# Performance work log

Hardware: AMD Instinct MI355X
Metric: run time of the kernel (lower is better)

Reference implementation:

```python
import jax, jax.numpy as jnp
import numpy as np

T, D, H = 65536, 256, 256


def setup_inputs() -> dict:
    key = jax.random.key(0)
    ks = jax.random.split(key, 6)
    lim = 1.0 / np.sqrt(H)  # equinox GRUCell init: U(-1/sqrt(hidden), 1/sqrt(hidden))
    x = jax.random.normal(ks[0], (T, D), dtype=jnp.float32)
    state = jnp.zeros((H,), dtype=jnp.float32)
    start = jax.random.randint(ks[1], (T,), 0, 2).astype(jnp.int32)  # episode-start mask
    next_done = jnp.zeros((T,), dtype=jnp.int32)  # unused by forward, kept for signature fidelity
    W_ih = jax.random.uniform(ks[2], (3 * H, D), minval=-lim, maxval=lim, dtype=jnp.float32)
    W_hh = jax.random.uniform(ks[3], (3 * H, H), minval=-lim, maxval=lim, dtype=jnp.float32)
    bias = jax.random.uniform(ks[4], (3 * H,), minval=-lim, maxval=lim, dtype=jnp.float32)
    bias_n = jax.random.uniform(ks[5], (H,), minval=-lim, maxval=lim, dtype=jnp.float32)
    return {"x": x, "state": state, "start": start, "next_done": next_done,
            "W_ih": W_ih, "W_hh": W_hh, "bias": bias, "bias_n": bias_n}


def reference(x, state, start, next_done, W_ih, W_hh, bias, bias_n):
    # Input-dependent gate pre-activations for all timesteps in one big GEMM: [T, 3H]
    igates_all = x @ W_ih.T + bias
    start_f = start.astype(x.dtype)

    def step(h, inp):
        ig, s = inp
        h = h * (1.0 - s)  # reset hidden at episode start (state * logical_not(start))
        hg = W_hh @ h  # [3H]
        r = jax.nn.sigmoid(ig[:H] + hg[:H])
        z = jax.nn.sigmoid(ig[H:2 * H] + hg[H:2 * H])
        n = jnp.tanh(ig[2 * H:] + r * (hg[2 * H:] + bias_n))
        new_h = n + z * (h - n)  # equinox GRUCell output
        return new_h, new_h

    final_state, y = jax.lax.scan(step, state, (igates_all, start_f))
    return y, final_state
```

## Files before the change

kernel.cpp:

```cpp
#include <hip/hip_runtime.h>
#include <hip/hip_bf16.h>
#include <stdint.h>

#define TT   65536
#define NCH  16
#define CNOM 16
#define NBLK 256
#define ROWB 1664

typedef __bf16 bf16x8 __attribute__((ext_vector_type(8)));
typedef float  f32x4  __attribute__((ext_vector_type(4)));
typedef int    i32x4  __attribute__((ext_vector_type(4)));

__device__ __bf16 g_wih[768 * 256];
__device__ __bf16 g_whh[768 * 256];
__device__ __bf16 g_xbf[TT * 256];
__device__ __align__(64) unsigned char g_ig[(size_t)TT * ROWB];

__device__ __forceinline__ void gl_lds16(const void* g, void* l) {
  __builtin_amdgcn_global_load_lds(
      (const __attribute__((address_space(1))) void*)(unsigned long long)(uintptr_t)g,
      (__attribute__((address_space(3))) void*)(unsigned int)(uintptr_t)l,
      16, 0, 0);
}

__device__ __forceinline__ bf16x8 as_bf16x8(i32x4 v) {
  bf16x8 r; __builtin_memcpy(&r, &v, 16); return r;
}
__device__ __forceinline__ float bfbits(uint32_t u) {
  float f; __builtin_memcpy(&f, &u, 4); return f;
}

__global__ void prep_w(const float* __restrict__ wih, const float* __restrict__ whh) {
  const int n = 768 * 256;
  for (int i = blockIdx.x * blockDim.x + threadIdx.x; i < n; i += gridDim.x * blockDim.x) {
    g_wih[i] = (__bf16)wih[i];
    g_whh[i] = (__bf16)whh[i];
  }
}

__global__ void prep_x(const float* __restrict__ x) {
  int i = (blockIdx.x * 256 + threadIdx.x) * 8;
  float4 a0 = *(const float4*)(x + i);
  float4 a1 = *(const float4*)(x + i + 4);
  bf16x8 v;
  v[0] = (__bf16)a0.x; v[1] = (__bf16)a0.y; v[2] = (__bf16)a0.z; v[3] = (__bf16)a0.w;
  v[4] = (__bf16)a1.x; v[5] = (__bf16)a1.y; v[6] = (__bf16)a1.z; v[7] = (__bf16)a1.w;
  *(bf16x8*)(g_xbf + i) = v;
}

__global__ __launch_bounds__(256) void gemm_ig(const float* __restrict__ bias) {
  __shared__ __align__(16) __bf16 a_s[128 * 64];
  __shared__ __align__(16) __bf16 b_s[128 * 64];
  const int tid = threadIdx.x;
  const int w = tid >> 6, lane = tid & 63, l15 = lane & 15, q = lane >> 4;
  const int mt = blockIdx.x / 6, ntb = blockIdx.x - mt * 6;
  const int m0 = mt * 128, n0 = ntb * 128;
  const int wm = w >> 1, wn = w & 1;

  f32x4 acc[4][4];
#pragma unroll
  for (int a = 0; a < 4; ++a)
#pragma unroll
    for (int b = 0; b < 4; ++b) acc[a][b] = (f32x4){0.f, 0.f, 0.f, 0.f};

  for (int kc = 0; kc < 4; ++kc) {
#pragma unroll
    for (int i = 0; i < 4; ++i) {
      int pslot = i * 256 + tid;
      int row = pslot >> 3, cb = (pslot & 7) ^ (row & 7);
      gl_lds16((const char*)g_xbf + ((size_t)(m0 + row) * 256 + kc * 64) * 2 + cb * 16,
               (char*)a_s + (i * 256 + (tid & ~63)) * 16);
      gl_lds16((const char*)g_wih + ((size_t)(n0 + row) * 256 + kc * 64) * 2 + cb * 16,
               (char*)b_s + (i * 256 + (tid & ~63)) * 16);
    }
    __syncthreads();
#pragma unroll
    for (int ks = 0; ks < 2; ++ks) {
      bf16x8 af[4], bfr[4];
#pragma unroll
      for (int tm = 0; tm < 4; ++tm) {
        int row = wm * 64 + tm * 16 + l15;
        int cb = (ks * 4 + q) ^ (row & 7);
        af[tm] = *(const bf16x8*)((const char*)a_s + row * 128 + cb * 16);
      }
#pragma unroll
      for (int tn = 0; tn < 4; ++tn) {
        int row = wn * 64 + tn * 16 + l15;
        int cb = (ks * 4 + q) ^ (row & 7);
        bfr[tn] = *(const bf16x8*)((const char*)b_s + row * 128 + cb * 16);
      }
#pragma unroll
      for (int tm = 0; tm < 4; ++tm)
#pragma unroll
        for (int tn = 0; tn < 4; ++tn)
          acc[tm][tn] = __builtin_amdgcn_mfma_f32_16x16x32_bf16(af[tm], bfr[tn], acc[tm][tn], 0, 0, 0);
    }
    __syncthreads();
  }
  float bv[4];
#pragma unroll
  for (int tn = 0; tn < 4; ++tn) bv[tn] = bias[n0 + wn * 64 + tn * 16 + l15];
#pragma unroll
  for (int tm = 0; tm < 4; ++tm) {
#pragma unroll
    for (int tp = 0; tp < 2; ++tp) {
#pragma unroll
      for (int r = 0; r < 4; ++r) {
        int t = m0 + wm * 64 + tm * 16 + q * 4 + r;
        __bf16 lo = (__bf16)(acc[tm][tp * 2][r] + bv[tp * 2]);
        __bf16 hi = (__bf16)(acc[tm][tp * 2 + 1][r] + bv[tp * 2 + 1]);
        unsigned short ulo, uhi;
        __builtin_memcpy(&ulo, &lo, 2); __builtin_memcpy(&uhi, &hi, 2);
        uint32_t u = (uint32_t)ulo | ((uint32_t)uhi << 16);
        *(uint32_t*)(g_ig + (size_t)t * ROWB + ntb * 256 + (wn * 2 + tp) * 64 + l15 * 4) = u;
      }
    }
  }
}

__global__ __launch_bounds__(512)
__attribute__((amdgpu_waves_per_eu(2, 2)))
void gru_scan(const float* __restrict__ state, const int* __restrict__ start,
              const float* __restrict__ bias_n, float* __restrict__ out) {
  __shared__ __align__(16) __bf16 h_s[2][16][264];
  __shared__ __align__(16) unsigned char whh_lds[8 * 16 * 1024];
  __shared__ int flg_s[16 * 132];
  __shared__ int s_arr[17];

  const int tid = threadIdx.x;
  const int w = tid >> 6, lane = tid & 63, l15 = lane & 15, q = lane >> 4;
  const int jrow0 = w * 32 + l15;

  if (tid < 17) {
    int t = (blockIdx.x * NCH + tid) * CNOM;
    if (t > 0) { while (t < TT && start[t] == 0) t++; }
    s_arr[tid] = t;
  }
  for (int i = tid; i < 16 * 264; i += 512) (&h_s[0][0][0])[i] = (__bf16)0.f;
  __syncthreads();

  int sa[4], len[4];
#pragma unroll
  for (int r = 0; r < 4; ++r) {
    sa[r] = s_arr[q * 4 + r];
    len[r] = s_arr[q * 4 + r + 1] - sa[r];
  }
  int ML = 0;
  for (int m = 0; m < 16; ++m) { int L = s_arr[m + 1] - s_arr[m]; ML = L > ML ? L : ML; }
  ML = __builtin_amdgcn_readfirstlane(ML);

  for (int idx = tid; idx < 2048; idx += 512) {
    int m = idx >> 7, kk = idx & 127;
    int t = s_arr[m] + kk;
    flg_s[m * 132 + kk] = (t < TT) ? start[t] : 0;
  }

  char* lp = (char*)whh_lds + w * 16384 + lane * 16;
#pragma unroll
  for (int p = 0; p < 2; ++p)
#pragma unroll
    for (int ks = 0; ks < 8; ++ks) {
      i32x4 t = *(const i32x4*)&g_whh[(size_t)(w * 32 + p * 16 + l15) * 256 + q * 8 + ks * 32];
      *(i32x4*)(lp + (p * 8 + ks) * 1024) = t;
    }
  i32x4 whh_r[2][2][8];
#pragma unroll
  for (int p = 0; p < 2; ++p)
#pragma unroll
    for (int c = 1; c < 3; ++c)
#pragma unroll
      for (int ks = 0; ks < 8; ++ks)
        whh_r[p][c - 1][ks] =
            *(const i32x4*)&g_whh[(size_t)(c * 256 + w * 32 + p * 16 + l15) * 256 + q * 8 + ks * 32];

  const float bn2[2] = { bias_n[jrow0], bias_n[jrow0 + 16] };

  const int start0 = start[0];
  if (blockIdx.x == 0 && tid < 256) h_s[0][0][tid] = start0 ? (__bf16)0.f : (__bf16)state[tid];

  float hreg[2][4];
#pragma unroll
  for (int p = 0; p < 2; ++p)
#pragma unroll
    for (int r = 0; r < 4; ++r) hreg[p][r] = 0.f;
  if (blockIdx.x == 0 && q == 0 && !start0) {
    hreg[0][0] = state[jrow0];
    hreg[1][0] = state[jrow0 + 16];
  }

  const int cw = (w >> 2) * 256 + ((w & 3) * 16 + l15) * 4;
  const uint32_t offlim = (uint32_t)(TT - 1) * ROWB + (uint32_t)cw;
  uint32_t off[4];
#pragma unroll
  for (int r = 0; r < 4; ++r) off[r] = (uint32_t)sa[r] * ROWB + (uint32_t)cw;

  const unsigned char* gig = g_ig;
  uint32_t igA[12], igB[12];
#pragma unroll
  for (int r = 0; r < 4; ++r) {
    igA[r * 3 + 0] = *(const uint32_t*)(gig + off[r]);
    igA[r * 3 + 1] = *(const uint32_t*)(gig + off[r] + 512);
    igA[r * 3 + 2] = *(const uint32_t*)(gig + off[r] + 1024);
    uint32_t nx = off[r] + ROWB; off[r] = nx > offlim ? offlim : nx;
  }
  __syncthreads();

  auto step = [&](int k, uint32_t (&cur)[12], uint32_t (&nxt)[12]) {
#pragma unroll
    for (int r = 0; r < 4; ++r) {
      nxt[r * 3 + 0] = *(const uint32_t*)(gig + off[r]);
      nxt[r * 3 + 1] = *(const uint32_t*)(gig + off[r] + 512);
      nxt[r * 3 + 2] = *(const uint32_t*)(gig + off[r] + 1024);
      uint32_t nx = off[r] + ROWB; off[r] = nx > offlim ? offlim : nx;
    }
    int fnext[4];
    if (k + 1 < 128) {
#pragma unroll
      for (int r = 0; r < 4; ++r) fnext[r] = flg_s[(q * 4 + r) * 132 + k + 1];
    } else {
#pragma unroll
      for (int r = 0; r < 4; ++r) {
        int t = sa[r] + k + 1; t = t > TT - 1 ? TT - 1 : t;
        fnext[r] = start[t];
      }
    }

    const __bf16* hb = &h_s[k & 1][0][0] + l15 * 264 + q * 8;
#pragma unroll
    for (int p = 0; p < 2; ++p) {
      f32x4 a0 = (f32x4){0.f, 0.f, 0.f, 0.f};
      f32x4 a1 = (f32x4){0.f, 0.f, 0.f, 0.f};
      f32x4 a2 = (f32x4){0.f, 0.f, 0.f, 0.f};
#pragma unroll
      for (int ks = 0; ks < 8; ++ks) {
        bf16x8 hf = *(const bf16x8*)(hb + ks * 32);
        i32x4 b0 = *(const i32x4*)(lp + (p * 8 + ks) * 1024);
        a0 = __builtin_amdgcn_mfma_f32_16x16x32_bf16(hf, as_bf16x8(b0), a0, 0, 0, 0);
        a1 = __builtin_amdgcn_mfma_f32_16x16x32_bf16(hf, as_bf16x8(whh_r[p][0][ks]), a1, 0, 0, 0);
        a2 = __builtin_amdgcn_mfma_f32_16x16x32_bf16(hf, as_bf16x8(whh_r[p][1][ks]), a2, 0, 0, 0);
      }
#pragma unroll
      for (int r = 0; r < 4; ++r) {
        uint32_t vr = cur[r * 3 + 0];
        uint32_t vz = cur[r * 3 + 1];
        uint32_t vn = cur[r * 3 + 2];
        float igr = bfbits(p ? (vr & 0xffff0000u) : (vr << 16));
        float igz = bfbits(p ? (vz & 0xffff0000u) : (vz << 16));
        float ign = bfbits(p ? (vn & 0xffff0000u) : (vn << 16));
        float rp_ = a0[r] + igr;
        float zp_ = a1[r] + igz;
        float hv  = a2[r] + bn2[p];
        float rg = 1.f / (1.f + __expf(-rp_));
        float zg = 1.f / (1.f + __expf(-zp_));
        float np = ign + rg * hv;
        np = fminf(fmaxf(np, -30.f), 30.f);
        float e2 = __expf(2.f * np);
        float ng = (e2 - 1.f) / (e2 + 1.f);
        float hn = ng + zg * (hreg[p][r] - ng);
        if (k < len[r]) out[(size_t)(sa[r] + k) * 256 + jrow0 + p * 16] = hn;
        hreg[p][r] = fnext[r] ? 0.f : hn;
      }
    }
    __bf16* hw = &h_s[(k + 1) & 1][0][0];
#pragma unroll
    for (int p = 0; p < 2; ++p)
#pragma unroll
      for (int r = 0; r < 4; ++r)
        hw[(q * 4 + r) * 264 + jrow0 + p * 16] = (__bf16)hreg[p][r];
    asm volatile("s_waitcnt lgkmcnt(0)" ::: "memory");
    __builtin_amdgcn_s_barrier();
  };

  for (int k = 0; k < ML; ) {
    step(k, igA, igB); ++k;
    if (k < ML) { step(k, igB, igA); ++k; }
  }
}

__global__ void fin_copy(float* __restrict__ out) {
  int i = threadIdx.x;
  out[(size_t)TT * 256 + i] = out[((size_t)TT - 1) * 256 + i];
}

extern "C" void kernel_launch(void* const* d_in, const int* in_sizes, int n_in,
                              void* d_out, int out_size, void* d_ws, size_t ws_size,
                              hipStream_t stream) {
  const float* x      = (const float*)d_in[0];
  const float* state  = (const float*)d_in[1];
  const int*   start  = (const int*)d_in[2];
  const float* wih    = (const float*)d_in[4];
  const float* whh    = (const float*)d_in[5];
  const float* bias   = (const float*)d_in[6];
  const float* bias_n = (const float*)d_in[7];
  float* out = (float*)d_out;

  prep_w<<<256, 256, 0, stream>>>(wih, whh);
  prep_x<<<8192, 256, 0, stream>>>(x);
  gemm_ig<<<3072, 256, 0, stream>>>(bias);
  gru_scan<<<NBLK, 512, 0, stream>>>(state, start, bias_n, out);
  fin_copy<<<1, 256, 0, stream>>>(out);
}
```

Measured before the change: 293.1 us.

## Fuse x bf16 conversion into GEMM and pin recurrent weights in AGPRs

Drops the separate prep_x kernel. The GEMM now loads fp32 x directly, converts it to bf16 in registers and stores it into the swizzled LDS tile, which avoids writing and rereading a bf16 copy of x. In the scan kernel, the z and n recurrent weight fragments are forced into AGPRs and fed to inline-asm MFMAs, with zero-init variants for the first k-step, to relieve VGPR pressure. Output addressing is changed to incrementing pointers. The hand-written asm brings fixed s_nop hazard padding and gives up compiler scheduling. The x load is now a synchronous register path instead of async global-to-LDS, and it is repeated by each of the 6 N-tile blocks.

```diff
diff --git a/kernel.cpp b/kernel.cpp
--- a/kernel.cpp
+++ b/kernel.cpp
@@ -14,7 +14,6 @@
 
 __device__ __bf16 g_wih[768 * 256];
 __device__ __bf16 g_whh[768 * 256];
-__device__ __bf16 g_xbf[TT * 256];
 __device__ __align__(64) unsigned char g_ig[(size_t)TT * ROWB];
 
 __device__ __forceinline__ void gl_lds16(const void* g, void* l) {
@@ -24,11 +23,21 @@
       16, 0, 0);
 }
 
-__device__ __forceinline__ bf16x8 as_bf16x8(i32x4 v) {
-  bf16x8 r; __builtin_memcpy(&r, &v, 16); return r;
-}
 __device__ __forceinline__ float bfbits(uint32_t u) {
   float f; __builtin_memcpy(&f, &u, 4); return f;
+}
+
+__device__ __forceinline__ void mfma_bv0(f32x4& acc, bf16x8 a, i32x4 b) {
+  asm("v_mfma_f32_16x16x32_bf16 %0, %1, %2, 0" : "=&v"(acc) : "v"(a), "v"(b));
+}
+__device__ __forceinline__ void mfma_ba0(f32x4& acc, bf16x8 a, i32x4 b) {
+  asm("v_mfma_f32_16x16x32_bf16 %0, %1, %2, 0" : "=&v"(acc) : "v"(a), "a"(b));
+}
+__device__ __forceinline__ void mfma_bv(f32x4& acc, bf16x8 a, i32x4 b) {
+  asm("v_mfma_f32_16x16x32_bf16 %0, %1, %2, %0" : "+v"(acc) : "v"(a), "v"(b));
+}
+__device__ __forceinline__ void mfma_ba(f32x4& acc, bf16x8 a, i32x4 b) {
+  asm("v_mfma_f32_16x16x32_bf16 %0, %1, %2, %0" : "+v"(acc) : "v"(a), "a"(b));
 }
 
 __global__ void prep_w(const float* __restrict__ wih, const float* __restrict__ whh) {
@@ -39,17 +48,8 @@
   }
 }
 
-__global__ void prep_x(const float* __restrict__ x) {
-  int i = (blockIdx.x * 256 + threadIdx.x) * 8;
-  float4 a0 = *(const float4*)(x + i);
-  float4 a1 = *(const float4*)(x + i + 4);
-  bf16x8 v;
-  v[0] = (__bf16)a0.x; v[1] = (__bf16)a0.y; v[2] = (__bf16)a0.z; v[3] = (__bf16)a0.w;
-  v[4] = (__bf16)a1.x; v[5] = (__bf16)a1.y; v[6] = (__bf16)a1.z; v[7] = (__bf16)a1.w;
-  *(bf16x8*)(g_xbf + i) = v;
-}
-
-__global__ __launch_bounds__(256) void gemm_ig(const float* __restrict__ bias) {
+__global__ __launch_bounds__(256) void gemm_ig(const float* __restrict__ x,
+                                               const float* __restrict__ bias) {
   __shared__ __align__(16) __bf16 a_s[128 * 64];
   __shared__ __align__(16) __bf16 b_s[128 * 64];
   const int tid = threadIdx.x;
@@ -68,10 +68,16 @@
 #pragma unroll
     for (int i = 0; i < 4; ++i) {
       int pslot = i * 256 + tid;
-      int row = pslot >> 3, cb = (pslot & 7) ^ (row & 7);
-      gl_lds16((const char*)g_xbf + ((size_t)(m0 + row) * 256 + kc * 64) * 2 + cb * 16,
-               (char*)a_s + (i * 256 + (tid & ~63)) * 16);
-      gl_lds16((const char*)g_wih + ((size_t)(n0 + row) * 256 + kc * 64) * 2 + cb * 16,
+      int row = pslot >> 3, c = pslot & 7;
+      int cs = c ^ (row & 7);
+      const float* xs = x + (size_t)(m0 + row) * 256 + kc * 64 + cs * 8;
+      float4 f0 = *(const float4*)xs;
+      float4 f1 = *(const float4*)(xs + 4);
+      bf16x8 v;
+      v[0] = (__bf16)f0.x; v[1] = (__bf16)f0.y; v[2] = (__bf16)f0.z; v[3] = (__bf16)f0.w;
+      v[4] = (__bf16)f1.x; v[5] = (__bf16)f1.y; v[6] = (__bf16)f1.z; v[7] = (__bf16)f1.w;
+      *(bf16x8*)((char*)a_s + pslot * 16) = v;
+      gl_lds16((const char*)g_wih + ((size_t)(n0 + row) * 256 + kc * 64) * 2 + cs * 16,
                (char*)b_s + (i * 256 + (tid & ~63)) * 16);
     }
     __syncthreads();
@@ -164,15 +170,21 @@
       i32x4 t = *(const i32x4*)&g_whh[(size_t)(w * 32 + p * 16 + l15) * 256 + q * 8 + ks * 32];
       *(i32x4*)(lp + (p * 8 + ks) * 1024) = t;
     }
-  i32x4 whh_r[2][2][8];
+  i32x4 whh_z[2][8], whh_n[2][8];
 #pragma unroll
   for (int p = 0; p < 2; ++p)
 #pragma unroll
-    for (int c = 1; c < 3; ++c)
-#pragma unroll
-      for (int ks = 0; ks < 8; ++ks)
-        whh_r[p][c - 1][ks] =
-            *(const i32x4*)&g_whh[(size_t)(c * 256 + w * 32 + p * 16 + l15) * 256 + q * 8 + ks * 32];
+    for (int ks = 0; ks < 8; ++ks) {
+      whh_z[p][ks] = *(const i32x4*)&g_whh[(size_t)(1 * 256 + w * 32 + p * 16 + l15) * 256 + q * 8 + ks * 32];
+      whh_n[p][ks] = *(const i32x4*)&g_whh[(size_t)(2 * 256 + w * 32 + p * 16 + l15) * 256 + q * 8 + ks * 32];
+    }
+#pragma unroll
+  for (int p = 0; p < 2; ++p)
+#pragma unroll
+    for (int ks = 0; ks < 8; ++ks) {
+      asm volatile("" : "+a"(whh_z[p][ks]));
+      asm volatile("" : "+a"(whh_n[p][ks]));
+    }
 
   const float bn2[2] = { bias_n[jrow0], bias_n[jrow0 + 16] };
 
@@ -192,8 +204,12 @@
   const int cw = (w >> 2) * 256 + ((w & 3) * 16 + l15) * 4;
   const uint32_t offlim = (uint32_t)(TT - 1) * ROWB + (uint32_t)cw;
   uint32_t off[4];
-#pragma unroll
-  for (int r = 0; r < 4; ++r) off[r] = (uint32_t)sa[r] * ROWB + (uint32_t)cw;
+  float* op[4];
+#pragma unroll
+  for (int r = 0; r < 4; ++r) {
+    off[r] = (uint32_t)sa[r] * ROWB + (uint32_t)cw;
+    op[r] = out + (size_t)sa[r] * 256 + jrow0;
+  }
 
   const unsigned char* gig = g_ig;
   uint32_t igA[12], igB[12];
@@ -229,17 +245,23 @@
     const __bf16* hb = &h_s[k & 1][0][0] + l15 * 264 + q * 8;
 #pragma unroll
     for (int p = 0; p < 2; ++p) {
-      f32x4 a0 = (f32x4){0.f, 0.f, 0.f, 0.f};
-      f32x4 a1 = (f32x4){0.f, 0.f, 0.f, 0.f};
-      f32x4 a2 = (f32x4){0.f, 0.f, 0.f, 0.f};
-#pragma unroll
-      for (int ks = 0; ks < 8; ++ks) {
+      f32x4 a0, a1, a2;
+      {
+        bf16x8 hf = *(const bf16x8*)(hb);
+        i32x4 b0 = *(const i32x4*)(lp + (p * 8) * 1024);
+        mfma_bv0(a0, hf, b0);
+        mfma_ba0(a1, hf, whh_z[p][0]);
+        mfma_ba0(a2, hf, whh_n[p][0]);
+      }
+#pragma unroll
+      for (int ks = 1; ks < 8; ++ks) {
         bf16x8 hf = *(const bf16x8*)(hb + ks * 32);
         i32x4 b0 = *(const i32x4*)(lp + (p * 8 + ks) * 1024);
-        a0 = __builtin_amdgcn_mfma_f32_16x16x32_bf16(hf, as_bf16x8(b0), a0, 0, 0, 0);
-        a1 = __builtin_amdgcn_mfma_f32_16x16x32_bf16(hf, as_bf16x8(whh_r[p][0][ks]), a1, 0, 0, 0);
-        a2 = __builtin_amdgcn_mfma_f32_16x16x32_bf16(hf, as_bf16x8(whh_r[p][1][ks]), a2, 0, 0, 0);
-      }
+        mfma_bv(a0, hf, b0);
+        mfma_ba(a1, hf, whh_z[p][ks]);
+        mfma_ba(a2, hf, whh_n[p][ks]);
+      }
+      asm volatile("s_nop 7\n\ts_nop 7" : "+v"(a0), "+v"(a1), "+v"(a2));
 #pragma unroll
       for (int r = 0; r < 4; ++r) {
         uint32_t vr = cur[r * 3 + 0];
@@ -258,7 +280,7 @@
         float e2 = __expf(2.f * np);
         float ng = (e2 - 1.f) / (e2 + 1.f);
         float hn = ng + zg * (hreg[p][r] - ng);
-        if (k < len[r]) out[(size_t)(sa[r] + k) * 256 + jrow0 + p * 16] = hn;
+        if (k < len[r]) op[r][p * 16] = hn;
         hreg[p][r] = fnext[r] ? 0.f : hn;
       }
     }
@@ -268,6 +290,8 @@
 #pragma unroll
       for (int r = 0; r < 4; ++r)
         hw[(q * 4 + r) * 264 + jrow0 + p * 16] = (__bf16)hreg[p][r];
+#pragma unroll
+    for (int r = 0; r < 4; ++r) op[r] += 256;
     asm volatile("s_waitcnt lgkmcnt(0)" ::: "memory");
     __builtin_amdgcn_s_barrier();
   };
@@ -296,8 +320,7 @@
   float* out = (float*)d_out;
 
   prep_w<<<256, 256, 0, stream>>>(wih, whh);
-  prep_x<<<8192, 256, 0, stream>>>(x);
-  gemm_ig<<<3072, 256, 0, stream>>>(bias);
+  gemm_ig<<<3072, 256, 0, stream>>>(x, bias);
   gru_scan<<<NBLK, 512, 0, stream>>>(state, start, bias_n, out);
   fin_copy<<<1, 256, 0, stream>>>(out);
 }
```

Result: slower. 304.0 us (+3.7%).
